# Kernel optimization log

Hardware: AMD Instinct MI355X
Metric: run time of the kernel (lower is better)

## Reference

```python
import jax, jax.numpy as jnp
import numpy as np

N_NODES = 50000
N_EDGES = 1600000
IN_CH, OUT_CH, SIZE = 128, 64, 4


def _segment_softmax(e, seg, n):
    # numerically stable softmax of edge scores grouped by segment id (PyG softmax)
    m = jax.ops.segment_max(e, seg, num_segments=n)
    ex = jnp.exp(e - m[seg])
    s = jax.ops.segment_sum(ex, seg, num_segments=n)
    return ex / (s[seg] + 1e-16)


def setup_inputs() -> dict:
    key = jax.random.key(0)
    k = jax.random.split(key, 6)
    x = jax.random.normal(k[0], (N_NODES, IN_CH), dtype=jnp.float32)
    edge_index = jax.random.randint(k[1], (2, N_EDGES), 0, N_NODES, dtype=jnp.int64)
    W = jax.random.normal(k[2], (SIZE, IN_CH, OUT_CH), dtype=jnp.float32) * 0.1
    att_src = jax.random.normal(k[3], (SIZE, OUT_CH), dtype=jnp.float32) * 0.1
    att_dst = jax.random.normal(k[4], (SIZE, OUT_CH), dtype=jnp.float32) * 0.1
    bias = jnp.zeros((SIZE, OUT_CH), dtype=jnp.float32)
    return {"x": x, "W": W, "att_src": att_src, "att_dst": att_dst,
            "bias": bias, "edge_index": edge_index, "direction": 1}


def reference(x, W, att_src, att_dst, bias, edge_index, direction):
    src, dst = edge_index[0], edge_index[1]
    n = x.shape[0]
    size = W.shape[0]
    feat_sum = None
    att_sum = None
    for i in range(size):  # small fixed ensemble of GATConv layers
        h = x @ W[i]                                    # [N, out]
        a_s = h @ att_src[i]                            # [N] source scores
        a_d = h @ att_dst[i]                            # [N] target scores
        e = jax.nn.leaky_relu(a_s[src] + a_d[dst], 0.2)  # [E] GAT slope 0.2
        alpha = _segment_softmax(e, dst, n)             # softmax over incoming edges
        out = jax.ops.segment_sum(alpha[:, None] * h[src], dst, num_segments=n) + bias[i]
        fl = jax.nn.leaky_relu(out, 0.01)               # f.leaky_relu default slope
        feat_sum = fl if feat_sum is None else feat_sum + fl
        att_sum = alpha if att_sum is None else att_sum + alpha
    # directional node pooling: mean of summed edge attention grouped by source node
    counts = jax.ops.segment_sum(jnp.ones_like(att_sum), src, num_segments=n)
    pooled = jax.ops.segment_sum(att_sum, src, num_segments=n) / jnp.maximum(counts, 1.0)
    node_scores = direction * pooled
    return feat_sum, node_scores
```

## Files before the change

### kernel.cpp

```cpp
#include <hip/hip_runtime.h>
#include <stdint.h>

#define N_NODES 50000
#define N_EDGES 1600000
#define IN_CH   128
#define OUT_CH  64
#define CAP     72
#define NBUCKET 196
#define MB      782
#define NODES48 (MB * 64)
#define EPB2    2047
#define BK2     40
#define NODES_PAD (NBUCKET * 256)
#define SENTINEL 0xFFFFFFFFu

typedef float  f32x4  __attribute__((ext_vector_type(4)));
typedef __bf16 bf16x8 __attribute__((ext_vector_type(8)));

__device__ __forceinline__ unsigned int f2bf(float f) {
    unsigned int u = __float_as_uint(f);
    u += 0x7fffu + ((u >> 16) & 1u);
    return u >> 16;
}
__device__ __forceinline__ float lrelu(float v, float s) { return v > 0.f ? v : s * v; }

__device__ __forceinline__ void split2(float f, unsigned short& hi, unsigned short& lo) {
    unsigned int u = __float_as_uint(f);
    hi = (unsigned short)(u >> 16);
    float r = f - __uint_as_float(u & 0xffff0000u);
    lo = (unsigned short)f2bf(r);
}

#define POOL_SCALE 268435456.0f
#define POOL_MASK  ((1ull << 40) - 1ull)

__global__ __launch_bounds__(256) void k_prep(
    const float* __restrict__ W, const float* __restrict__ att_src,
    const float* __restrict__ att_dst,
    unsigned short* __restrict__ Wh, unsigned short* __restrict__ Wl,
    float* __restrict__ w_s, float* __restrict__ w_d)
{
    const int l = blockIdx.x;
    const int tid = threadIdx.x;
    const float* Wb = W + (size_t)l * IN_CH * OUT_CH;

    for (int idx = tid; idx < IN_CH * OUT_CH; idx += 256) {
        int c = idx >> 7, k = idx & 127;
        unsigned short h, lo2;
        split2(Wb[k * OUT_CH + c], h, lo2);
        Wh[l * 8192 + idx] = h;
        Wl[l * 8192 + idx] = lo2;
    }
    if (tid < IN_CH) {
        float s = 0.f, d = 0.f;
        const float* As = att_src + l * OUT_CH;
        const float* Ad = att_dst + l * OUT_CH;
        const float* wr = Wb + tid * OUT_CH;
#pragma unroll 8
        for (int c = 0; c < OUT_CH; ++c) { s = fmaf(wr[c], As[c], s); d = fmaf(wr[c], Ad[c], d); }
        w_s[l * IN_CH + tid] = s;
        w_d[l * IN_CH + tid] = d;
    }
}

__global__ __launch_bounds__(256) void k_front(
    const float* __restrict__ x, const float* __restrict__ w_s,
    const float* __restrict__ w_d,
    unsigned int* __restrict__ X16, float* __restrict__ a_s, float* __restrict__ a_d,
    const int* __restrict__ ei, unsigned int* __restrict__ binned2,
    int* __restrict__ cnt2)
{
    __shared__ int lcnt[NBUCKET];
    __shared__ unsigned int stage[BK2 * 256];

    const int tid  = threadIdx.x;
    const int lane = tid & 63;
    const int q    = lane & 31;
    const int h    = lane >> 5;
    const int wv   = __builtin_amdgcn_readfirstlane(tid >> 6);
    const int blk  = blockIdx.x;
    const int row0 = blk * 64;

    {
        const float4* ws4 = (const float4*)w_s;
        const float4* wd4 = (const float4*)w_d;
        float4 rs0 = ws4[q], rs1 = ws4[32 + q], rs2 = ws4[64 + q], rs3 = ws4[96 + q];
        float4 rd0 = wd4[q], rd1 = wd4[32 + q], rd2 = wd4[64 + q], rd3 = wd4[96 + q];
#pragma unroll 2
        for (int r = 0; r < 8; ++r) {
            int node = row0 + wv * 16 + 2 * r + h;
            float4 xv = make_float4(0.f, 0.f, 0.f, 0.f);
            if (node < N_NODES)
                xv = ((const float4*)(x + (size_t)node * IN_CH))[q];
            if (node < N_NODES) {
                uint2 pk;
                pk.x = f2bf(xv.x) | (f2bf(xv.y) << 16);
                pk.y = f2bf(xv.z) | (f2bf(xv.w) << 16);
                ((uint2*)(X16 + (size_t)node * 64))[q] = pk;
            }
            float s0 = xv.x*rs0.x + xv.y*rs0.y + xv.z*rs0.z + xv.w*rs0.w;
            float s1 = xv.x*rs1.x + xv.y*rs1.y + xv.z*rs1.z + xv.w*rs1.w;
            float s2 = xv.x*rs2.x + xv.y*rs2.y + xv.z*rs2.z + xv.w*rs2.w;
            float s3 = xv.x*rs3.x + xv.y*rs3.y + xv.z*rs3.z + xv.w*rs3.w;
            float d0 = xv.x*rd0.x + xv.y*rd0.y + xv.z*rd0.z + xv.w*rd0.w;
            float d1 = xv.x*rd1.x + xv.y*rd1.y + xv.z*rd1.z + xv.w*rd1.w;
            float d2 = xv.x*rd2.x + xv.y*rd2.y + xv.z*rd2.z + xv.w*rd2.w;
            float d3 = xv.x*rd3.x + xv.y*rd3.y + xv.z*rd3.z + xv.w*rd3.w;
#pragma unroll
            for (int off = 1; off <= 16; off <<= 1) {
                s0 += __shfl_xor(s0, off); s1 += __shfl_xor(s1, off);
                s2 += __shfl_xor(s2, off); s3 += __shfl_xor(s3, off);
                d0 += __shfl_xor(d0, off); d1 += __shfl_xor(d1, off);
                d2 += __shfl_xor(d2, off); d3 += __shfl_xor(d3, off);
            }
            if (q == 0 && node < N_NODES) {
                ((float4*)a_s)[node] = make_float4(s0, s1, s2, s3);
                ((float4*)a_d)[node] = make_float4(d0, d1, d2, d3);
            }
        }
    }

    const int start = blk * EPB2;
    const int end = (start + EPB2 < N_EDGES) ? start + EPB2 : N_EDGES;

    int probe = ei[2 * (start + tid) + 1];
    const int is64 = (__ballot(probe != 0) == 0ull) ? 1 : 0;

    for (int i = tid; i < NBUCKET; i += 256) lcnt[i] = 0;
    __syncthreads();

    if (is64) {
        const int2* e2 = (const int2*)ei;
        for (int e = start + tid; e < end; e += 256) {
            int s = e2[e].x;
            int d = e2[(size_t)N_EDGES + e].x;
            int bk = d >> 8;
            unsigned int pk = ((unsigned int)s << 16) | (unsigned int)d;
            int pos = atomicAdd(&lcnt[bk], 1);
            if (pos < BK2) stage[pos * 256 + bk] = pk;
        }
    } else {
        for (int e = start + tid; e < end; e += 256) {
            int s = ei[e];
            int d = ei[N_EDGES + e];
            int bk = d >> 8;
            unsigned int pk = ((unsigned int)s << 16) | (unsigned int)d;
            int pos = atomicAdd(&lcnt[bk], 1);
            if (pos < BK2) stage[pos * 256 + bk] = pk;
        }
    }
    __syncthreads();

    if (tid < NBUCKET) {
        int c = lcnt[tid];
        if (c > BK2) c = BK2;
        cnt2[(size_t)tid * MB + blk] = c;
        uint4* dstp = (uint4*)(binned2 + ((size_t)tid * MB + blk) * BK2);
        for (int p = 0; p < c; p += 4) {
            uint4 v;
            v.x = stage[p * 256 + tid];
            v.y = (p + 1 < c) ? stage[(p + 1) * 256 + tid] : SENTINEL;
            v.z = (p + 2 < c) ? stage[(p + 2) * 256 + tid] : SENTINEL;
            v.w = (p + 3 < c) ? stage[(p + 3) * 256 + tid] : SENTINEL;
            dstp[p >> 2] = v;
        }
    }
}

__global__ __launch_bounds__(1024) void k_bucket(
    const unsigned int* __restrict__ binned2, const int* __restrict__ cnt2,
    unsigned short* __restrict__ slot, int* __restrict__ cnt_dst,
    unsigned long long* __restrict__ pool)
{
    __shared__ unsigned short sl[256 * CAP];
    __shared__ int cnt[256];
    const int b = blockIdx.x;
    const int tid = threadIdx.x;
    if (tid < 256) cnt[tid] = 0;
    int pidx = b * 1024 + tid;
    if (pidx < N_NODES) pool[pidx] = 0ull;
    __syncthreads();

    if (tid < MB) {
        int c = cnt2[(size_t)b * MB + tid];
        if (c > BK2) c = BK2;
        const uint4* cp = (const uint4*)(binned2 + ((size_t)b * MB + tid) * BK2);
        for (int p = 0; p < c; p += 4) {
            uint4 v = cp[p >> 2];
            {
                unsigned int pk = v.x; int local = pk & 255;
                int pos = atomicAdd(&cnt[local], 1);
                if (pos < CAP) sl[local * CAP + pos] = (unsigned short)(pk >> 16);
            }
            if (p + 1 < c) {
                unsigned int pk = v.y; int local = pk & 255;
                int pos = atomicAdd(&cnt[local], 1);
                if (pos < CAP) sl[local * CAP + pos] = (unsigned short)(pk >> 16);
            }
            if (p + 2 < c) {
                unsigned int pk = v.z; int local = pk & 255;
                int pos = atomicAdd(&cnt[local], 1);
                if (pos < CAP) sl[local * CAP + pos] = (unsigned short)(pk >> 16);
            }
            if (p + 3 < c) {
                unsigned int pk = v.w; int local = pk & 255;
                int pos = atomicAdd(&cnt[local], 1);
                if (pos < CAP) sl[local * CAP + pos] = (unsigned short)(pk >> 16);
            }
        }
    }
    __syncthreads();

    uint4* g = (uint4*)(slot + (size_t)b * 256 * CAP);
    const uint4* l = (const uint4*)sl;
    for (int i = tid; i < 256 * CAP * 2 / 16; i += 1024) g[i] = l[i];
    if (tid < 256) cnt_dst[b * 256 + tid] = cnt[tid];
}

__global__ __launch_bounds__(256) void k_gather(
    const unsigned int* __restrict__ X16, const unsigned short* __restrict__ slot,
    const int* __restrict__ cnt_dst,
    const float* __restrict__ a_s, const float* __restrict__ a_d,
    unsigned long long* __restrict__ pool, unsigned int* __restrict__ AG)
{
    __shared__ __align__(16) float ewlds[4][CAP * 4];

    const int lane = threadIdx.x & 63;
    const int wv = __builtin_amdgcn_readfirstlane(threadIdx.x >> 6);
    const int node = blockIdx.x * 4 + wv;
    int deg = __builtin_amdgcn_readfirstlane(cnt_dst[node]);
    if (deg > CAP) deg = CAP;
    float* ewl = ewlds[wv];

    const float4* as4p = (const float4*)a_s;
    const unsigned short* s16 = slot + (size_t)node * CAP;
    const float4 ad4 = ((const float4*)a_d)[node];

    float se0 = 0.f, se1 = 0.f, se2 = 0.f, se3 = 0.f;
#pragma unroll
    for (int base = 0; base < CAP; base += 64) {
        int j = base + lane;
        if (j < deg) {
            int s = s16[j];
            float4 as4 = as4p[s];
            float t0 = as4.x + ad4.x, t1 = as4.y + ad4.y;
            float t2 = as4.z + ad4.z, t3 = as4.w + ad4.w;
            float4 e4;
            e4.x = __expf(fmaxf(t0, 0.2f * t0));
            e4.y = __expf(fmaxf(t1, 0.2f * t1));
            e4.z = __expf(fmaxf(t2, 0.2f * t2));
            e4.w = __expf(fmaxf(t3, 0.2f * t3));
            *(float4*)(ewl + j * 4) = e4;
            se0 += e4.x; se1 += e4.y; se2 += e4.z; se3 += e4.w;
        }
    }
#pragma unroll
    for (int off = 1; off <= 32; off <<= 1) {
        se0 += __shfl_xor(se0, off); se1 += __shfl_xor(se1, off);
        se2 += __shfl_xor(se2, off); se3 += __shfl_xor(se3, off);
    }
    const float i0 = 1.0f / (se0 + 1e-16f);
    const float i1 = 1.0f / (se1 + 1e-16f);
    const float i2 = 1.0f / (se2 + 1e-16f);
    const float i3 = 1.0f / (se3 + 1e-16f);

    float a00 = 0.f, a01 = 0.f, a10 = 0.f, a11 = 0.f;
    float a20 = 0.f, a21 = 0.f, a30 = 0.f, a31 = 0.f;
    const unsigned int* Xp = X16 + lane;

    auto body = [&](unsigned int s, int j) {
        float4 e4 = *(const float4*)(ewl + j * 4);
        unsigned int xv = Xp[(size_t)s * 64];
        float x0 = __uint_as_float(xv << 16);
        float x1 = __uint_as_float(xv & 0xffff0000u);
        a00 = fmaf(e4.x, x0, a00); a01 = fmaf(e4.x, x1, a01);
        a10 = fmaf(e4.y, x0, a10); a11 = fmaf(e4.y, x1, a11);
        a20 = fmaf(e4.z, x0, a20); a21 = fmaf(e4.z, x1, a21);
        a30 = fmaf(e4.w, x0, a30); a31 = fmaf(e4.w, x1, a31);
    };

    const unsigned int* sp = (const unsigned int*)s16;
    const int npair = deg >> 1;
    int j2 = 0;
    for (; j2 + 8 <= npair; j2 += 8) {
        uint4 pa = *(const uint4*)(sp + j2);
        uint4 pb = *(const uint4*)(sp + j2 + 4);
        body(pa.x & 0xffffu, 2*j2+0); body(pa.x >> 16, 2*j2+1);
        body(pa.y & 0xffffu, 2*j2+2); body(pa.y >> 16, 2*j2+3);
        body(pa.z & 0xffffu, 2*j2+4); body(pa.z >> 16, 2*j2+5);
        body(pa.w & 0xffffu, 2*j2+6); body(pa.w >> 16, 2*j2+7);
        body(pb.x & 0xffffu, 2*j2+8); body(pb.x >> 16, 2*j2+9);
        body(pb.y & 0xffffu, 2*j2+10); body(pb.y >> 16, 2*j2+11);
        body(pb.z & 0xffffu, 2*j2+12); body(pb.z >> 16, 2*j2+13);
        body(pb.w & 0xffffu, 2*j2+14); body(pb.w >> 16, 2*j2+15);
    }
    for (; j2 + 4 <= npair; j2 += 4) {
        uint4 p4 = *(const uint4*)(sp + j2);
        body(p4.x & 0xffffu, 2*j2+0); body(p4.x >> 16, 2*j2+1);
        body(p4.y & 0xffffu, 2*j2+2); body(p4.y >> 16, 2*j2+3);
        body(p4.z & 0xffffu, 2*j2+4); body(p4.z >> 16, 2*j2+5);
        body(p4.w & 0xffffu, 2*j2+6); body(p4.w >> 16, 2*j2+7);
    }
    for (; j2 < npair; ++j2) {
        unsigned int pr = sp[j2];
        body(pr & 0xffffu, 2*j2); body(pr >> 16, 2*j2+1);
    }
    if (deg & 1) body(sp[npair] & 0xffffu, deg - 1);

    unsigned int* agp = AG + ((size_t)node * 4) * 64 + lane;
    agp[0]   = f2bf(a00 * i0) | (f2bf(a01 * i0) << 16);
    agp[64]  = f2bf(a10 * i1) | (f2bf(a11 * i1) << 16);
    agp[128] = f2bf(a20 * i2) | (f2bf(a21 * i2) << 16);
    agp[192] = f2bf(a30 * i3) | (f2bf(a31 * i3) << 16);

    for (int jj = lane; jj < deg; jj += 64) {
        int s = s16[jj];
        float4 e4 = *(const float4*)(ewl + jj * 4);
        float tot = e4.x * i0 + e4.y * i1 + e4.z * i2 + e4.w * i3;
        unsigned long long enc = (1ull << 40) |
            (unsigned long long)(tot * POOL_SCALE + 0.5f);
        atomicAdd(pool + s, enc);
    }
}

__global__ __launch_bounds__(256) void k_out(
    const unsigned short* __restrict__ AG, const unsigned short* __restrict__ Wh,
    const unsigned short* __restrict__ Wl, const float* __restrict__ bias,
    const unsigned long long* __restrict__ pool, const int* __restrict__ dirp,
    float* __restrict__ out)
{
    const int tid = threadIdx.x;
    const int lane = tid & 63;
    const int lr = lane & 15, lg = lane >> 4;
    const int wv = __builtin_amdgcn_readfirstlane(tid >> 6);
    const int row0 = blockIdx.x * 64;

    f32x4 fsum[4];
#pragma unroll
    for (int n = 0; n < 4; ++n) fsum[n] = (f32x4){0.f, 0.f, 0.f, 0.f};

#pragma unroll 1
    for (int l = 0; l < 4; ++l) {
        f32x4 acc[4];
#pragma unroll
        for (int n = 0; n < 4; ++n) acc[n] = (f32x4){0.f, 0.f, 0.f, 0.f};
        const unsigned short* Whl = Wh + l * 8192;
        const unsigned short* Wll = Wl + l * 8192;
#pragma unroll
        for (int ks = 0; ks < 4; ++ks) {
            size_t node = row0 + wv * 16 + lr;
            bf16x8 a = *(const bf16x8*)(AG + (node * 4 + l) * 128 + ks * 32 + lg * 8);
#pragma unroll
            for (int n = 0; n < 4; ++n) {
                int offw = (n * 16 + lr) * 128 + ks * 32 + lg * 8;
                bf16x8 bhi = *(const bf16x8*)(Whl + offw);
                bf16x8 blo = *(const bf16x8*)(Wll + offw);
                acc[n] = __builtin_amdgcn_mfma_f32_16x16x32_bf16(a, bhi, acc[n], 0, 0, 0);
                acc[n] = __builtin_amdgcn_mfma_f32_16x16x32_bf16(a, blo, acc[n], 0, 0, 0);
            }
        }
#pragma unroll
        for (int n = 0; n < 4; ++n) {
            float bn = bias[l * OUT_CH + n * 16 + lr];
#pragma unroll
            for (int qq = 0; qq < 4; ++qq)
                fsum[n][qq] += lrelu(acc[n][qq] + bn, 0.01f);
        }
    }

#pragma unroll
    for (int n = 0; n < 4; ++n)
#pragma unroll
        for (int qq = 0; qq < 4; ++qq) {
            int node = row0 + wv * 16 + lg * 4 + qq;
            if (node < N_NODES)
                out[(size_t)node * 64 + n * 16 + lr] = fsum[n][qq];
        }

    if (tid < 64) {
        int node = row0 + tid;
        if (node < N_NODES) {
            unsigned long long v = pool[node];
            unsigned int cnt = (unsigned int)(v >> 40);
            float val = (float)((double)(v & POOL_MASK) * (1.0 / (double)POOL_SCALE));
            int di = dirp[0];
            float dirf = (di >= -1000 && di <= 1000) ? (float)di : __int_as_float(di);
            float denom = (cnt > 1u) ? (float)cnt : 1.0f;
            out[(size_t)N_NODES * 64 + node] = dirf * val / denom;
        }
    }
}

extern "C" void kernel_launch(void* const* d_in, const int* in_sizes, int n_in,
                              void* d_out, int out_size, void* d_ws, size_t ws_size,
                              hipStream_t stream)
{
    const float* x       = (const float*)d_in[0];
    const float* W       = (const float*)d_in[1];
    const float* att_src = (const float*)d_in[2];
    const float* att_dst = (const float*)d_in[3];
    const float* bias    = (const float*)d_in[4];
    const int*   ei      = (const int*)d_in[5];
    const int*   dirp    = (const int*)d_in[6];
    float* out = (float*)d_out;

    char* w = (char*)d_ws;
    size_t off = 0;
    auto alloc = [&](size_t bytes) -> void* {
        void* p = w + off;
        off = (off + bytes + 255) & ~(size_t)255;
        return p;
    };
    unsigned long long* pool = (unsigned long long*)alloc((size_t)N_NODES * sizeof(unsigned long long));
    float* a_s = (float*)alloc((size_t)N_NODES * 4 * sizeof(float));
    float* a_d = (float*)alloc((size_t)N_NODES * 4 * sizeof(float));
    int* cnt_dst = (int*)alloc((size_t)NODES_PAD * sizeof(int));
    unsigned short* slot = (unsigned short*)alloc((size_t)NODES_PAD * CAP * sizeof(unsigned short));
    unsigned int* X16 = (unsigned int*)alloc((size_t)NODES48 * 64 * sizeof(unsigned int));
    unsigned short* Wh = (unsigned short*)alloc((size_t)4 * 8192 * sizeof(unsigned short));
    unsigned short* Wl = (unsigned short*)alloc((size_t)4 * 8192 * sizeof(unsigned short));
    float* w_s = (float*)alloc((size_t)4 * IN_CH * sizeof(float));
    float* w_d = (float*)alloc((size_t)4 * IN_CH * sizeof(float));
    int* cnt2 = (int*)alloc((size_t)NBUCKET * MB * sizeof(int));
    unsigned short* AG = (unsigned short*)alloc((size_t)NODES48 * 4 * IN_CH * sizeof(unsigned short));
    unsigned int* binned2 = (unsigned int*)AG;
    (void)ws_size; (void)in_sizes; (void)n_in; (void)out_size;

    k_prep<<<4, 256, 0, stream>>>(W, att_src, att_dst, Wh, Wl, w_s, w_d);
    k_front<<<MB, 256, 0, stream>>>(x, w_s, w_d, X16, a_s, a_d, ei, binned2, cnt2);
    k_bucket<<<NBUCKET, 1024, 0, stream>>>(binned2, cnt2, slot, cnt_dst, pool);
    k_gather<<<N_NODES / 4, 256, 0, stream>>>(X16, slot, cnt_dst, a_s, a_d, pool,
                                              (unsigned int*)AG);
    k_out<<<MB, 256, 0, stream>>>(AG, Wh, Wl, bias, pool, dirp, out);
}
```

Baseline: 286.9 us.

## Replace two-pass LDS bucketing with direct global-atomic CSR slot fill

Removes the separate bucketing kernel and its staged binned intermediate buffer. Each edge now does a global atomicAdd on its destination counter and writes the source id straight into that destination's slot row, using a grid-stride kernel that also zeroes pool and computes the node projections. This saves one launch and a round trip through global memory. The cost is 1.6M contended global atomics plus scattered 2-byte writes, and an extra memset of the counters. Slot order within each node also becomes nondeterministic.

```diff
diff --git a/kernel.cpp b/kernel.cpp
--- a/kernel.cpp
+++ b/kernel.cpp
@@ -6,13 +6,10 @@
 #define IN_CH   128
 #define OUT_CH  64
 #define CAP     72
-#define NBUCKET 196
 #define MB      782
 #define NODES48 (MB * 64)
-#define EPB2    2047
-#define BK2     40
-#define NODES_PAD (NBUCKET * 256)
-#define SENTINEL 0xFFFFFFFFu
+#define NODES_PAD 50176
+#define FGRID   2048
 
 typedef float  f32x4  __attribute__((ext_vector_type(4)));
 typedef __bf16 bf16x8 __attribute__((ext_vector_type(8)));
@@ -63,25 +60,24 @@
     }
 }
 
-__global__ __launch_bounds__(256) void k_front(
+__global__ __launch_bounds__(256) void k_frontier(
     const float* __restrict__ x, const float* __restrict__ w_s,
     const float* __restrict__ w_d,
     unsigned int* __restrict__ X16, float* __restrict__ a_s, float* __restrict__ a_d,
-    const int* __restrict__ ei, unsigned int* __restrict__ binned2,
-    int* __restrict__ cnt2)
-{
-    __shared__ int lcnt[NBUCKET];
-    __shared__ unsigned int stage[BK2 * 256];
-
+    const int* __restrict__ ei, int* __restrict__ cnt_dst,
+    unsigned short* __restrict__ slot, unsigned long long* __restrict__ pool)
+{
     const int tid  = threadIdx.x;
     const int lane = tid & 63;
     const int q    = lane & 31;
     const int h    = lane >> 5;
     const int wv   = __builtin_amdgcn_readfirstlane(tid >> 6);
-    const int blk  = blockIdx.x;
-    const int row0 = blk * 64;
-
-    {
+
+    for (int i = blockIdx.x * 256 + tid; i < N_NODES; i += FGRID * 256)
+        pool[i] = 0ull;
+
+    for (int nt = blockIdx.x; nt < MB; nt += FGRID) {
+        const int row0 = nt * 64;
         const float4* ws4 = (const float4*)w_s;
         const float4* wd4 = (const float4*)w_d;
         float4 rs0 = ws4[q], rs1 = ws4[32 + q], rs2 = ws4[64 + q], rs3 = ws4[96 + q];
@@ -120,101 +116,25 @@
         }
     }
 
-    const int start = blk * EPB2;
-    const int end = (start + EPB2 < N_EDGES) ? start + EPB2 : N_EDGES;
-
-    int probe = ei[2 * (start + tid) + 1];
+    int probe = ei[2 * tid + 1];
     const int is64 = (__ballot(probe != 0) == 0ull) ? 1 : 0;
-
-    for (int i = tid; i < NBUCKET; i += 256) lcnt[i] = 0;
-    __syncthreads();
 
     if (is64) {
         const int2* e2 = (const int2*)ei;
-        for (int e = start + tid; e < end; e += 256) {
+        for (int e = blockIdx.x * 256 + tid; e < N_EDGES; e += FGRID * 256) {
             int s = e2[e].x;
             int d = e2[(size_t)N_EDGES + e].x;
-            int bk = d >> 8;
-            unsigned int pk = ((unsigned int)s << 16) | (unsigned int)d;
-            int pos = atomicAdd(&lcnt[bk], 1);
-            if (pos < BK2) stage[pos * 256 + bk] = pk;
+            int pos = atomicAdd(&cnt_dst[d], 1);
+            if (pos < CAP) slot[(size_t)d * CAP + pos] = (unsigned short)s;
         }
     } else {
-        for (int e = start + tid; e < end; e += 256) {
+        for (int e = blockIdx.x * 256 + tid; e < N_EDGES; e += FGRID * 256) {
             int s = ei[e];
             int d = ei[N_EDGES + e];
-            int bk = d >> 8;
-            unsigned int pk = ((unsigned int)s << 16) | (unsigned int)d;
-            int pos = atomicAdd(&lcnt[bk], 1);
-            if (pos < BK2) stage[pos * 256 + bk] = pk;
-        }
-    }
-    __syncthreads();
-
-    if (tid < NBUCKET) {
-        int c = lcnt[tid];
-        if (c > BK2) c = BK2;
-        cnt2[(size_t)tid * MB + blk] = c;
-        uint4* dstp = (uint4*)(binned2 + ((size_t)tid * MB + blk) * BK2);
-        for (int p = 0; p < c; p += 4) {
-            uint4 v;
-            v.x = stage[p * 256 + tid];
-            v.y = (p + 1 < c) ? stage[(p + 1) * 256 + tid] : SENTINEL;
-            v.z = (p + 2 < c) ? stage[(p + 2) * 256 + tid] : SENTINEL;
-            v.w = (p + 3 < c) ? stage[(p + 3) * 256 + tid] : SENTINEL;
-            dstp[p >> 2] = v;
-        }
-    }
-}
-
-__global__ __launch_bounds__(1024) void k_bucket(
-    const unsigned int* __restrict__ binned2, const int* __restrict__ cnt2,
-    unsigned short* __restrict__ slot, int* __restrict__ cnt_dst,
-    unsigned long long* __restrict__ pool)
-{
-    __shared__ unsigned short sl[256 * CAP];
-    __shared__ int cnt[256];
-    const int b = blockIdx.x;
-    const int tid = threadIdx.x;
-    if (tid < 256) cnt[tid] = 0;
-    int pidx = b * 1024 + tid;
-    if (pidx < N_NODES) pool[pidx] = 0ull;
-    __syncthreads();
-
-    if (tid < MB) {
-        int c = cnt2[(size_t)b * MB + tid];
-        if (c > BK2) c = BK2;
-        const uint4* cp = (const uint4*)(binned2 + ((size_t)b * MB + tid) * BK2);
-        for (int p = 0; p < c; p += 4) {
-            uint4 v = cp[p >> 2];
-            {
-                unsigned int pk = v.x; int local = pk & 255;
-                int pos = atomicAdd(&cnt[local], 1);
-                if (pos < CAP) sl[local * CAP + pos] = (unsigned short)(pk >> 16);
-            }
-            if (p + 1 < c) {
-                unsigned int pk = v.y; int local = pk & 255;
-                int pos = atomicAdd(&cnt[local], 1);
-                if (pos < CAP) sl[local * CAP + pos] = (unsigned short)(pk >> 16);
-            }
-            if (p + 2 < c) {
-                unsigned int pk = v.z; int local = pk & 255;
-                int pos = atomicAdd(&cnt[local], 1);
-                if (pos < CAP) sl[local * CAP + pos] = (unsigned short)(pk >> 16);
-            }
-            if (p + 3 < c) {
-                unsigned int pk = v.w; int local = pk & 255;
-                int pos = atomicAdd(&cnt[local], 1);
-                if (pos < CAP) sl[local * CAP + pos] = (unsigned short)(pk >> 16);
-            }
-        }
-    }
-    __syncthreads();
-
-    uint4* g = (uint4*)(slot + (size_t)b * 256 * CAP);
-    const uint4* l = (const uint4*)sl;
-    for (int i = tid; i < 256 * CAP * 2 / 16; i += 1024) g[i] = l[i];
-    if (tid < 256) cnt_dst[b * 256 + tid] = cnt[tid];
+            int pos = atomicAdd(&cnt_dst[d], 1);
+            if (pos < CAP) slot[(size_t)d * CAP + pos] = (unsigned short)s;
+        }
+    }
 }
 
 __global__ __launch_bounds__(256) void k_gather(
@@ -421,14 +341,13 @@
     unsigned short* Wl = (unsigned short*)alloc((size_t)4 * 8192 * sizeof(unsigned short));
     float* w_s = (float*)alloc((size_t)4 * IN_CH * sizeof(float));
     float* w_d = (float*)alloc((size_t)4 * IN_CH * sizeof(float));
-    int* cnt2 = (int*)alloc((size_t)NBUCKET * MB * sizeof(int));
     unsigned short* AG = (unsigned short*)alloc((size_t)NODES48 * 4 * IN_CH * sizeof(unsigned short));
-    unsigned int* binned2 = (unsigned int*)AG;
     (void)ws_size; (void)in_sizes; (void)n_in; (void)out_size;
 
+    hipMemsetAsync(cnt_dst, 0, (size_t)NODES_PAD * sizeof(int), stream);
     k_prep<<<4, 256, 0, stream>>>(W, att_src, att_dst, Wh, Wl, w_s, w_d);
-    k_front<<<MB, 256, 0, stream>>>(x, w_s, w_d, X16, a_s, a_d, ei, binned2, cnt2);
-    k_bucket<<<NBUCKET, 1024, 0, stream>>>(binned2, cnt2, slot, cnt_dst, pool);
+    k_frontier<<<FGRID, 256, 0, stream>>>(x, w_s, w_d, X16, a_s, a_d, ei,
+                                          cnt_dst, slot, pool);
     k_gather<<<N_NODES / 4, 256, 0, stream>>>(X16, slot, cnt_dst, a_s, a_d, pool,
                                               (unsigned int*)AG);
     k_out<<<MB, 256, 0, stream>>>(AG, Wh, Wl, bias, pool, dirp, out);
```

Measured after the change: 346.5 us. 1.21x slower.

## Shrink per-block bucket staging with global overflow list and pre-swizzle MFMA weight fragments

Applied to the files above, without the earlier changes.

Per-block bucket staging capacity drops from 40 to 24 entries, which cuts shared memory in k_front (allowing more resident blocks) and shrinks the binned2 traffic. Edges beyond the smaller capacity now spill to a global overflow list that every k_bucket block scans, which also keeps edges that the old code silently dropped. Separately, the split hi/lo bf16 weights are laid out in per-lane MFMA fragment order, so k_out reads contiguous 16-byte chunks per lane. The risks are contention on the single global atomic counter and the cost of each of the 196 k_bucket blocks scanning the whole overflow list.

```diff
diff --git a/kernel.cpp b/kernel.cpp
--- a/kernel.cpp
+++ b/kernel.cpp
@@ -10,7 +10,8 @@
 #define MB      782
 #define NODES48 (MB * 64)
 #define EPB2    2047
-#define BK2     40
+#define BK2     24
+#define GOVF_CAP 8192
 #define NODES_PAD (NBUCKET * 256)
 #define SENTINEL 0xFFFFFFFFu
 
@@ -37,19 +38,30 @@
 __global__ __launch_bounds__(256) void k_prep(
     const float* __restrict__ W, const float* __restrict__ att_src,
     const float* __restrict__ att_dst,
-    unsigned short* __restrict__ Wh, unsigned short* __restrict__ Wl,
-    float* __restrict__ w_s, float* __restrict__ w_d)
+    unsigned short* __restrict__ Wp,
+    float* __restrict__ w_s, float* __restrict__ w_d, int* __restrict__ gcnt)
 {
     const int l = blockIdx.x;
     const int tid = threadIdx.x;
     const float* Wb = W + (size_t)l * IN_CH * OUT_CH;
 
-    for (int idx = tid; idx < IN_CH * OUT_CH; idx += 256) {
-        int c = idx >> 7, k = idx & 127;
-        unsigned short h, lo2;
-        split2(Wb[k * OUT_CH + c], h, lo2);
-        Wh[l * 8192 + idx] = h;
-        Wl[l * 8192 + idx] = lo2;
+    for (int idx = tid; idx < 16 * 2 * 64; idx += 256) {
+        int lane2 = idx & 63;
+        int h2 = (idx >> 6) & 1;
+        int f2 = idx >> 7;
+        int ks = f2 >> 2, n = f2 & 3;
+        int lg = lane2 >> 4, lr = lane2 & 15;
+        unsigned short fr[8];
+#pragma unroll
+        for (int j = 0; j < 8; ++j) {
+            int k = ks * 32 + lg * 8 + j;
+            int c = n * 16 + lr;
+            unsigned short hi, lo2;
+            split2(Wb[k * OUT_CH + c], hi, lo2);
+            fr[j] = h2 ? lo2 : hi;
+        }
+        *(uint4*)(Wp + (((size_t)l * 16 + f2) * 2 + h2) * 512 + lane2 * 8) =
+            *(const uint4*)fr;
     }
     if (tid < IN_CH) {
         float s = 0.f, d = 0.f;
@@ -61,6 +73,7 @@
         w_s[l * IN_CH + tid] = s;
         w_d[l * IN_CH + tid] = d;
     }
+    if (l == 0 && tid == 0) gcnt[0] = 0;
 }
 
 __global__ __launch_bounds__(256) void k_front(
@@ -68,7 +81,7 @@
     const float* __restrict__ w_d,
     unsigned int* __restrict__ X16, float* __restrict__ a_s, float* __restrict__ a_d,
     const int* __restrict__ ei, unsigned int* __restrict__ binned2,
-    int* __restrict__ cnt2)
+    int* __restrict__ cnt2, int* __restrict__ gcnt, unsigned int* __restrict__ govf)
 {
     __shared__ int lcnt[NBUCKET];
     __shared__ unsigned int stage[BK2 * 256];
@@ -138,6 +151,10 @@
             unsigned int pk = ((unsigned int)s << 16) | (unsigned int)d;
             int pos = atomicAdd(&lcnt[bk], 1);
             if (pos < BK2) stage[pos * 256 + bk] = pk;
+            else {
+                int gi = atomicAdd(gcnt, 1);
+                if (gi < GOVF_CAP) { govf[2 * gi] = (unsigned int)bk; govf[2 * gi + 1] = pk; }
+            }
         }
     } else {
         for (int e = start + tid; e < end; e += 256) {
@@ -147,6 +164,10 @@
             unsigned int pk = ((unsigned int)s << 16) | (unsigned int)d;
             int pos = atomicAdd(&lcnt[bk], 1);
             if (pos < BK2) stage[pos * 256 + bk] = pk;
+            else {
+                int gi = atomicAdd(gcnt, 1);
+                if (gi < GOVF_CAP) { govf[2 * gi] = (unsigned int)bk; govf[2 * gi + 1] = pk; }
+            }
         }
     }
     __syncthreads();
@@ -169,6 +190,7 @@
 
 __global__ __launch_bounds__(1024) void k_bucket(
     const unsigned int* __restrict__ binned2, const int* __restrict__ cnt2,
+    const int* __restrict__ gcnt, const unsigned int* __restrict__ govf,
     unsigned short* __restrict__ slot, int* __restrict__ cnt_dst,
     unsigned long long* __restrict__ pool)
 {
@@ -204,6 +226,18 @@
             }
             if (p + 3 < c) {
                 unsigned int pk = v.w; int local = pk & 255;
+                int pos = atomicAdd(&cnt[local], 1);
+                if (pos < CAP) sl[local * CAP + pos] = (unsigned short)(pk >> 16);
+            }
+        }
+    }
+    {
+        int nov = gcnt[0];
+        if (nov > GOVF_CAP) nov = GOVF_CAP;
+        for (int i = tid; i < nov; i += 1024) {
+            if ((int)govf[2 * i] == b) {
+                unsigned int pk = govf[2 * i + 1];
+                int local = pk & 255;
                 int pos = atomicAdd(&cnt[local], 1);
                 if (pos < CAP) sl[local * CAP + pos] = (unsigned short)(pk >> 16);
             }
@@ -324,8 +358,8 @@
 }
 
 __global__ __launch_bounds__(256) void k_out(
-    const unsigned short* __restrict__ AG, const unsigned short* __restrict__ Wh,
-    const unsigned short* __restrict__ Wl, const float* __restrict__ bias,
+    const unsigned short* __restrict__ AG, const unsigned short* __restrict__ Wp,
+    const float* __restrict__ bias,
     const unsigned long long* __restrict__ pool, const int* __restrict__ dirp,
     float* __restrict__ out)
 {
@@ -344,17 +378,16 @@
         f32x4 acc[4];
 #pragma unroll
         for (int n = 0; n < 4; ++n) acc[n] = (f32x4){0.f, 0.f, 0.f, 0.f};
-        const unsigned short* Whl = Wh + l * 8192;
-        const unsigned short* Wll = Wl + l * 8192;
 #pragma unroll
         for (int ks = 0; ks < 4; ++ks) {
             size_t node = row0 + wv * 16 + lr;
             bf16x8 a = *(const bf16x8*)(AG + (node * 4 + l) * 128 + ks * 32 + lg * 8);
 #pragma unroll
             for (int n = 0; n < 4; ++n) {
-                int offw = (n * 16 + lr) * 128 + ks * 32 + lg * 8;
-                bf16x8 bhi = *(const bf16x8*)(Whl + offw);
-                bf16x8 blo = *(const bf16x8*)(Wll + offw);
+                const unsigned short* fb =
+                    Wp + (((size_t)l * 16 + ks * 4 + n) * 2) * 512 + lane * 8;
+                bf16x8 bhi = *(const bf16x8*)(fb);
+                bf16x8 blo = *(const bf16x8*)(fb + 512);
                 acc[n] = __builtin_amdgcn_mfma_f32_16x16x32_bf16(a, bhi, acc[n], 0, 0, 0);
                 acc[n] = __builtin_amdgcn_mfma_f32_16x16x32_bf16(a, blo, acc[n], 0, 0, 0);
             }
@@ -417,19 +450,21 @@
     int* cnt_dst = (int*)alloc((size_t)NODES_PAD * sizeof(int));
     unsigned short* slot = (unsigned short*)alloc((size_t)NODES_PAD * CAP * sizeof(unsigned short));
     unsigned int* X16 = (unsigned int*)alloc((size_t)NODES48 * 64 * sizeof(unsigned int));
-    unsigned short* Wh = (unsigned short*)alloc((size_t)4 * 8192 * sizeof(unsigned short));
-    unsigned short* Wl = (unsigned short*)alloc((size_t)4 * 8192 * sizeof(unsigned short));
+    unsigned short* Wp = (unsigned short*)alloc((size_t)4 * 16 * 2 * 512 * sizeof(unsigned short));
     float* w_s = (float*)alloc((size_t)4 * IN_CH * sizeof(float));
     float* w_d = (float*)alloc((size_t)4 * IN_CH * sizeof(float));
     int* cnt2 = (int*)alloc((size_t)NBUCKET * MB * sizeof(int));
+    int* gcnt = (int*)alloc(256);
+    unsigned int* govf = (unsigned int*)alloc((size_t)2 * GOVF_CAP * sizeof(unsigned int));
     unsigned short* AG = (unsigned short*)alloc((size_t)NODES48 * 4 * IN_CH * sizeof(unsigned short));
     unsigned int* binned2 = (unsigned int*)AG;
     (void)ws_size; (void)in_sizes; (void)n_in; (void)out_size;
 
-    k_prep<<<4, 256, 0, stream>>>(W, att_src, att_dst, Wh, Wl, w_s, w_d);
-    k_front<<<MB, 256, 0, stream>>>(x, w_s, w_d, X16, a_s, a_d, ei, binned2, cnt2);
-    k_bucket<<<NBUCKET, 1024, 0, stream>>>(binned2, cnt2, slot, cnt_dst, pool);
+    k_prep<<<4, 256, 0, stream>>>(W, att_src, att_dst, Wp, w_s, w_d, gcnt);
+    k_front<<<MB, 256, 0, stream>>>(x, w_s, w_d, X16, a_s, a_d, ei, binned2, cnt2,
+                                    gcnt, govf);
+    k_bucket<<<NBUCKET, 1024, 0, stream>>>(binned2, cnt2, gcnt, govf, slot, cnt_dst, pool);
     k_gather<<<N_NODES / 4, 256, 0, stream>>>(X16, slot, cnt_dst, a_s, a_d, pool,
                                               (unsigned int*)AG);
-    k_out<<<MB, 256, 0, stream>>>(AG, Wh, Wl, bias, pool, dirp, out);
-}
+    k_out<<<MB, 256, 0, stream>>>(AG, Wp, bias, pool, dirp, out);
+}
```

Result: faster. 236.2 us (-17.7%).
